# Performance work log

Measured on AMD Instinct MI355X. Metric: run time of the kernel, lower is better.

Reference implementation:

```python
import jax, jax.numpy as jnp
import numpy as np

T, D_IN, D_OUT, R, S = 8192, 4096, 4096, 16, 16  # tokens, in, out, lora rank, n_stacks
GATE_THRESHOLD = 0.12


def setup_inputs() -> dict:
    key = jax.random.key(0)
    ks = jax.random.split(key, 6)
    x = jax.random.normal(ks[0], (T, D_IN), jnp.float32)
    W = jax.random.normal(ks[1], (D_OUT, D_IN), jnp.float32) * 0.02  # frozen linear weight
    b = jax.random.normal(ks[2], (D_OUT,), jnp.float32) * 0.02       # frozen linear bias
    A = jax.random.normal(ks[3], (S, R, D_IN), jnp.float32) * 0.02   # per-stack lora_A
    B = jax.random.normal(ks[4], (S, D_OUT, R), jnp.float32) * 0.02  # per-stack lora_B
    domain_weights = jax.random.uniform(ks[5], (S,), jnp.float32)    # sigmoid-router weights per domain
    stack_domain = jnp.arange(S, dtype=jnp.int32)                    # stack -> domain index (count=1 each)
    return {"x": x, "W": W, "b": b, "A": A, "B": B,
            "domain_weights": domain_weights, "stack_domain": stack_domain}


def reference(x, W, b, A, B, domain_weights, stack_domain):
    # base frozen linear: out = x @ W^T + b
    base = x @ W.T + b  # [T, D_OUT]
    # threshold-gated per-stack weights: w if w > GATE_THRESHOLD else 0
    g = jnp.where(domain_weights > GATE_THRESHOLD, domain_weights, 0.0)[stack_domain]  # [S]
    # grouped LoRA: stack(x) = (x @ A_s^T) @ B_s^T, combined with gate weights
    h = jnp.einsum('td,srd->str', x, A)          # [S, T, R]
    lora = jnp.einsum('s,str,sor->to', g, h, B)  # [T, D_OUT]
    # original wraps stack contributions in torch.no_grad()
    return base + jax.lax.stop_gradient(lora)
```

## Files before the change

kernel.cpp:

```cpp
#include <hip/hip_runtime.h>
#include <hip/hip_bf16.h>

typedef __bf16 bf16;
typedef __attribute__((ext_vector_type(8))) __bf16 bf16x8;
typedef __attribute__((ext_vector_type(4))) float f32x4;

#define T_TOK 8192
#define DIN   4096
#define DOUT  4096
#define RNK   16
#define NS    16
#define KLORA (NS * RNK)
#define GATE  0.12f

typedef __attribute__((address_space(1))) const void gconst_t;
typedef __attribute__((address_space(3))) void lds_t;

__device__ __forceinline__ void gload_lds16(const void* g, void* l) {
  __builtin_amdgcn_global_load_lds((gconst_t*)g, (lds_t*)l, 16, 0, 0);
}

#define BAR() do { asm volatile("" ::: "memory"); \
                   __builtin_amdgcn_s_barrier();  \
                   asm volatile("" ::: "memory"); } while (0)
#define VMW(n) asm volatile("s_waitcnt vmcnt(" #n ")" ::: "memory")


__global__ __launch_bounds__(256)
void cast_x_kernel(const float* __restrict__ x, bf16* __restrict__ xb) {
  const long i = ((long)blockIdx.x * 256 + threadIdx.x) * 8;
  const float4 v0 = *(const float4*)(x + i);
  const float4 v1 = *(const float4*)(x + i + 4);
  bf16x8 o;
  o[0] = (bf16)v0.x; o[1] = (bf16)v0.y; o[2] = (bf16)v0.z; o[3] = (bf16)v0.w;
  o[4] = (bf16)v1.x; o[5] = (bf16)v1.y; o[6] = (bf16)v1.z; o[7] = (bf16)v1.w;
  *(bf16x8*)(xb + i) = o;
}

__global__ __launch_bounds__(256)
void build_bg_kernel(const float* __restrict__ B, const float* __restrict__ dw,
                     const int* __restrict__ sd, bf16* __restrict__ bg) {
  const int t = blockIdx.x * 256 + threadIdx.x;
  const int o = t >> 8, k = t & 255, s = k >> 4, r = k & 15;
  const float w = dw[sd[s]];
  const float g = (w > GATE) ? w : 0.f;
  bg[t] = (bf16)(g * B[((size_t)s * DOUT + o) * RNK + r]);
}

__global__ __launch_bounds__(256)
void transpose_a_kernel(const float* __restrict__ A, bf16* __restrict__ at) {
  __shared__ float t[32][33];
  const int d0 = blockIdx.x * 32, k0 = blockIdx.y * 32;
  const int tx = threadIdx.x & 31, ty = threadIdx.x >> 5;
#pragma unroll
  for (int i = 0; i < 32; i += 8)
    t[ty + i][tx] = A[(size_t)(k0 + ty + i) * DIN + d0 + tx];
  __syncthreads();
#pragma unroll
  for (int i = 0; i < 32; i += 8)
    at[(size_t)(d0 + ty + i) * KLORA + k0 + tx] = (bf16)t[tx][ty + i];
}

__global__ __launch_bounds__(256)
void gemm_bt(const bf16* __restrict__ Am, const bf16* __restrict__ Bm,
             const float* __restrict__ extra, bf16* __restrict__ outB,
             int M, int N, int K) {
  constexpr int BM = 128, BN = 128, BK = 32;
  __shared__ __align__(16) bf16 At[BM * BK];
  __shared__ __align__(16) bf16 Bt[BN * BK];

  const int tid  = threadIdx.x;
  const int wave = tid >> 6, lane = tid & 63;

  const int nwg = gridDim.x, bid = blockIdx.x;
  const int qq  = nwg >> 3;
  const int sw  = (bid & 7) * qq + (bid >> 3);
  const int ntN = N / BN;
  const long row0 = (long)(sw / ntN) * BM;
  const long col0 = (long)(sw % ntN) * BN;

  f32x4 acc[4][4] = {};
  const int kSteps = K / BK;

  auto stage = [&](int ks) {
    const long k0 = (long)ks * BK;
#pragma unroll
    for (int r = 0; r < 2; ++r) {
      const int off = tid * 16 + r * 4096;
      const int row = off >> 6;
      const int el  = (off & 63) >> 1;
      char* ldsA = (char*)At + (wave << 10) + (r << 12);
      char* ldsB = (char*)Bt + (wave << 10) + (r << 12);
      gload_lds16(Am + (row0 + row) * K + k0 + el, ldsA);
      gload_lds16(Bm + (col0 + row) * K + k0 + el, ldsB);
    }
  };

  stage(0);
  for (int ks = 0; ks < kSteps; ++ks) {
    __syncthreads();
    bf16x8 afr[4], bfr[4];
    const int koff = (lane >> 4) << 3;
    const int rsel = lane & 15;
    const int wr = wave >> 1, wc = wave & 1;
#pragma unroll
    for (int m = 0; m < 4; ++m)
      afr[m] = *(const bf16x8*)&At[((wr << 6) + (m << 4) + rsel) * BK + koff];
#pragma unroll
    for (int n = 0; n < 4; ++n)
      bfr[n] = *(const bf16x8*)&Bt[((wc << 6) + (n << 4) + rsel) * BK + koff];
    __syncthreads();
    if (ks + 1 < kSteps) stage(ks + 1);
#pragma unroll
    for (int m = 0; m < 4; ++m)
#pragma unroll
      for (int n = 0; n < 4; ++n)
        acc[m][n] = __builtin_amdgcn_mfma_f32_16x16x32_bf16(afr[m], bfr[n],
                                                            acc[m][n], 0, 0, 0);
  }

  const int wr = wave >> 1, wc = wave & 1;
#pragma unroll
  for (int m = 0; m < 4; ++m)
#pragma unroll
    for (int n = 0; n < 4; ++n)
#pragma unroll
      for (int j = 0; j < 4; ++j) {
        const long row = row0 + wr * 64 + m * 16 + ((lane >> 4) << 2) + j;
        const long col = col0 + wc * 64 + n * 16 + (lane & 15);
        outB[row * N + col] = (bf16)(acc[m][n][j] + extra[row * N + col]);
      }
}

__global__ __launch_bounds__(512, 2)
void gemm256(const bf16* __restrict__ Am, const bf16* __restrict__ Bm,
             const float* __restrict__ bias, float* __restrict__ out,
             int M, int N, int K) {
  extern __shared__ char smem[];
  const int tid  = threadIdx.x;
  const int wave = tid >> 6, lane = tid & 63;
  const int wr = wave >> 2, wc = wave & 3;
  const int rsel = lane & 15, klane = lane >> 4;

  const int nwg = gridDim.x, bid = blockIdx.x;
  const int sw  = (bid & 7) * (nwg >> 3) + (bid >> 3);
  const int ntN = N >> 8;
  const long row0 = (long)(sw / ntN) << 8;
  const long col0 = (long)(sw % ntN) << 8;

  long srcA[2], srcB[2];
  int  ldsd[2];
#pragma unroll
  for (int r = 0; r < 2; ++r) {
    const int beta = ((wave * 2 + r) << 10) + (lane << 4);
    const int row  = ((beta >> 7) << 1) | (((beta >> 6) ^ (beta >> 8)) & 1);
    const int kb   = (beta & 0x30) ^ ((row & 1) << 4) ^ (((row >> 1) & 1) << 5);
    srcA[r] = (row0 + row) * (long)K + (kb >> 1);
    srcB[r] = (col0 + row) * (long)K + (kb >> 1);
    ldsd[r] = (wave * 2 + r) << 10;
  }

  auto stageA = [&](int t1, int s, int slot) {
    const long kofs = (long)t1 * 64 + s * 32;
#pragma unroll
    for (int r = 0; r < 2; ++r)
      gload_lds16(Am + srcA[r] + kofs, smem + (slot << 14) + ldsd[r]);
  };
  auto stageB = [&](int t1, int s, int slot) {
    const long kofs = (long)t1 * 64 + s * 32;
#pragma unroll
    for (int r = 0; r < 2; ++r)
      gload_lds16(Bm + srcB[r] + kofs, smem + (slot << 14) + ldsd[r]);
  };

  const int laneoff = (rsel << 6) ^ (klane << 4) ^ ((rsel & 7) << 4);

  f32x4 acc[8][4] = {};
  bf16x8 afr[4], bfr[4];

  auto readA = [&](int p, int s, int mh) {
    const char* base = smem + ((4 * p + 2 * s) << 14)
                            + ((wr * 128 + mh * 64) << 6) + laneoff;
#pragma unroll
    for (int mi = 0; mi < 4; ++mi)
      afr[mi] = *(const bf16x8*)(base + (mi << 10));
  };
  auto readB = [&](int p, int s) {
    const char* base = smem + ((4 * p + 2 * s + 1) << 14)
                            + ((wc * 64) << 6) + laneoff;
#pragma unroll
    for (int n = 0; n < 4; ++n)
      bfr[n] = *(const bf16x8*)(base + (n << 10));
  };
  auto mfma16 = [&](int mh) {
    __builtin_amdgcn_s_setprio(1);
#pragma unroll
    for (int mi = 0; mi < 4; ++mi)
#pragma unroll
      for (int n = 0; n < 4; ++n)
        acc[mh * 4 + mi][n] = __builtin_amdgcn_mfma_f32_16x16x32_bf16(
            afr[mi], bfr[n], acc[mh * 4 + mi][n], 0, 0, 0);
    __builtin_amdgcn_s_setprio(0);
  };

  const int nT = K >> 6;

  stageA(0, 0, 0); stageB(0, 0, 1); stageA(0, 1, 2); stageB(0, 1, 3);
  VMW(4);
  BAR();

  for (int t = 0; t < nT; ++t) {
    const int p = t & 1, q = p ^ 1;
    const bool pf = (t + 1 < nT);
    readB(p, 0); readA(p, 0, 0);
    if (pf) stageA(t + 1, 0, 4 * q + 0);
    BAR();
    mfma16(0);
    BAR();
    readA(p, 0, 1);
    if (pf) stageB(t + 1, 0, 4 * q + 1);
    BAR();
    mfma16(1);
    if (pf) { VMW(4); } else { VMW(0); }
    BAR();
    readB(p, 1); readA(p, 1, 0);
    if (pf) stageA(t + 1, 1, 4 * q + 2);
    BAR();
    mfma16(0);
    BAR();
    readA(p, 1, 1);
    if (pf) stageB(t + 1, 1, 4 * q + 3);
    BAR();
    mfma16(1);
    if (pf) { VMW(4); } else { VMW(0); }
    BAR();
  }

#pragma unroll
  for (int m = 0; m < 8; ++m)
#pragma unroll
    for (int n = 0; n < 4; ++n)
#pragma unroll
      for (int j = 0; j < 4; ++j) {
        const long row = row0 + wr * 128 + m * 16 + klane * 4 + j;
        const long col = col0 + wc * 64 + n * 16 + rsel;
        out[row * N + col] = acc[m][n][j] + bias[col];
      }
}


extern "C" void kernel_launch(void* const* d_in, const int* in_sizes, int n_in,
                              void* d_out, int out_size, void* d_ws, size_t ws_size,
                              hipStream_t stream) {
  (void)in_sizes; (void)n_in; (void)out_size; (void)ws_size;
  const float* x  = (const float*)d_in[0];
  const float* W  = (const float*)d_in[1];
  const float* b  = (const float*)d_in[2];
  const float* A  = (const float*)d_in[3];
  const float* B  = (const float*)d_in[4];
  const float* dw = (const float*)d_in[5];
  const int*   sd = (const int*)d_in[6];
  float* out = (float*)d_out;

  char* ws = (char*)d_ws;
  bf16* xb    = (bf16*)(ws);
  bf16* weff  = (bf16*)(ws + ((size_t)64 << 20));
  bf16* bg    = (bf16*)(ws + ((size_t)96 << 20));
  bf16* acatT = (bf16*)(ws + ((size_t)98 << 20));

  cast_x_kernel<<<(T_TOK * DIN / 8) / 256, 256, 0, stream>>>(x, xb);
  build_bg_kernel<<<(DOUT * KLORA) / 256, 256, 0, stream>>>(B, dw, sd, bg);
  transpose_a_kernel<<<dim3(DIN / 32, KLORA / 32), 256, 0, stream>>>(A, acatT);

  gemm_bt<<<(DOUT / 128) * (DIN / 128), 256, 0, stream>>>(
      bg, acatT, W, weff, DOUT, DIN, KLORA);

  static_assert((T_TOK % 256) == 0 && (DOUT % 256) == 0 && (DIN % 64) == 0, "");
  hipFuncSetAttribute(reinterpret_cast<const void*>(gemm256),
                      hipFuncAttributeMaxDynamicSharedMemorySize, 131072);
  gemm256<<<(T_TOK / 256) * (DOUT / 256), 512, 131072, stream>>>(
      xb, weff, b, out, T_TOK, DOUT, DIN);
}
```

Baseline: 344.4 us.

## Deepen GEMM LDS prefetch pipeline and simplify swizzle layout

```diff
diff --git a/kernel.cpp b/kernel.cpp
--- a/kernel.cpp
+++ b/kernel.cpp
@@ -150,44 +150,48 @@
 
   long srcA[2], srcB[2];
   int  ldsd[2];
-#pragma unroll
-  for (int r = 0; r < 2; ++r) {
-    const int beta = ((wave * 2 + r) << 10) + (lane << 4);
-    const int row  = ((beta >> 7) << 1) | (((beta >> 6) ^ (beta >> 8)) & 1);
-    const int kb   = (beta & 0x30) ^ ((row & 1) << 4) ^ (((row >> 1) & 1) << 5);
-    srcA[r] = (row0 + row) * (long)K + (kb >> 1);
-    srcB[r] = (col0 + row) * (long)K + (kb >> 1);
-    ldsd[r] = (wave * 2 + r) << 10;
+  {
+    const int rlo = lane >> 2;
+    const int kbe = (((lane & 3) * 16) ^ (((lane >> 5) & 1) << 5)) >> 1;
+#pragma unroll
+    for (int r = 0; r < 2; ++r) {
+      const int row = wave * 32 + r * 16 + rlo;
+      srcA[r] = (row0 + row) * (long)K + kbe;
+      srcB[r] = (col0 + row) * (long)K + kbe;
+      ldsd[r] = (wave * 2 + r) << 10;
+    }
   }
 
-  auto stageA = [&](int t1, int s, int slot) {
-    const long kofs = (long)t1 * 64 + s * 32;
-#pragma unroll
-    for (int r = 0; r < 2; ++r)
-      gload_lds16(Am + srcA[r] + kofs, smem + (slot << 14) + ldsd[r]);
-  };
-  auto stageB = [&](int t1, int s, int slot) {
-    const long kofs = (long)t1 * 64 + s * 32;
-#pragma unroll
-    for (int r = 0; r < 2; ++r)
-      gload_lds16(Bm + srcB[r] + kofs, smem + (slot << 14) + ldsd[r]);
-  };
-
-  const int laneoff = (rsel << 6) ^ (klane << 4) ^ ((rsel & 7) << 4);
+  const int nT = K >> 6;
+
+  auto stage_half = [&](int H) {
+    if (H >= 4 * nT) return;
+    const int  slot = H & 7;
+    const long kofs = (long)(H >> 2) * 64 + (long)((H >> 1) & 1) * 32;
+    if (H & 1) {
+#pragma unroll
+      for (int r = 0; r < 2; ++r)
+        gload_lds16(Bm + srcB[r] + kofs, smem + (slot << 14) + ldsd[r]);
+    } else {
+#pragma unroll
+      for (int r = 0; r < 2; ++r)
+        gload_lds16(Am + srcA[r] + kofs, smem + (slot << 14) + ldsd[r]);
+    }
+  };
+
+  const int laneoff = rsel * 64 + ((klane * 16) ^ ((rsel & 8) << 2));
 
   f32x4 acc[8][4] = {};
   bf16x8 afr[4], bfr[4];
 
-  auto readA = [&](int p, int s, int mh) {
-    const char* base = smem + ((4 * p + 2 * s) << 14)
-                            + ((wr * 128 + mh * 64) << 6) + laneoff;
+  auto readA = [&](int slot, int mh) {
+    const char* base = smem + (slot << 14) + ((wr * 128 + mh * 64) << 6) + laneoff;
 #pragma unroll
     for (int mi = 0; mi < 4; ++mi)
       afr[mi] = *(const bf16x8*)(base + (mi << 10));
   };
-  auto readB = [&](int p, int s) {
-    const char* base = smem + ((4 * p + 2 * s + 1) << 14)
-                            + ((wc * 64) << 6) + laneoff;
+  auto readB = [&](int slot) {
+    const char* base = smem + (slot << 14) + ((wc * 64) << 6) + laneoff;
 #pragma unroll
     for (int n = 0; n < 4; ++n)
       bfr[n] = *(const bf16x8*)(base + (n << 10));
@@ -203,36 +207,27 @@
     __builtin_amdgcn_s_setprio(0);
   };
 
-  const int nT = K >> 6;
-
-  stageA(0, 0, 0); stageB(0, 0, 1); stageA(0, 1, 2); stageB(0, 1, 3);
+  stage_half(0); stage_half(1); stage_half(2); stage_half(3);
   VMW(4);
+  stage_half(4); stage_half(5); stage_half(6);
+  VMW(6);
   BAR();
 
   for (int t = 0; t < nT; ++t) {
-    const int p = t & 1, q = p ^ 1;
-    const bool pf = (t + 1 < nT);
-    readB(p, 0); readA(p, 0, 0);
-    if (pf) stageA(t + 1, 0, 4 * q + 0);
-    BAR();
-    mfma16(0);
-    BAR();
-    readA(p, 0, 1);
-    if (pf) stageB(t + 1, 0, 4 * q + 1);
-    BAR();
-    mfma16(1);
-    if (pf) { VMW(4); } else { VMW(0); }
-    BAR();
-    readB(p, 1); readA(p, 1, 0);
-    if (pf) stageA(t + 1, 1, 4 * q + 2);
-    BAR();
-    mfma16(0);
-    BAR();
-    readA(p, 1, 1);
-    if (pf) stageB(t + 1, 1, 4 * q + 3);
-    BAR();
-    mfma16(1);
-    if (pf) { VMW(4); } else { VMW(0); }
+    const int b = (t & 1) << 2;
+    readB(b | 1); readA(b | 0, 0);
+    stage_half(4 * t + 7);
+    BAR(); mfma16(0); BAR();
+    readA(b | 0, 1);
+    stage_half(4 * t + 8);
+    BAR(); mfma16(1); BAR();
+    readB(b | 3); readA(b | 2, 0);
+    stage_half(4 * t + 9);
+    BAR(); mfma16(0); BAR();
+    readA(b | 2, 1);
+    stage_half(4 * t + 10);
+    BAR(); mfma16(1);
+    if (t == nT - 2) { VMW(0); } else { VMW(6); }
     BAR();
   }
 
```

New measurement: 329.5 us. 4.3% less time.
